# Optimization experiments

Hardware: AMD Instinct MI355X
Metric: run time of the kernel (lower is better)

## Reference

```python
import jax, jax.numpy as jnp
import numpy as np


def setup_inputs() -> dict:
    key = jax.random.key(0)
    ks = jax.random.split(key, 7)
    B, S, D, H = 8, 1024, 1024, 16
    dk = D // H
    return {
        "q": jax.random.normal(ks[0], (B, S, D), dtype=jnp.float32),
        "k": jax.random.normal(ks[1], (B, S, D), dtype=jnp.float32),
        "v": jax.random.normal(ks[2], (B, S, D), dtype=jnp.float32),
        "Wq": jax.random.normal(ks[3], (H, dk, D), dtype=jnp.float32) * 0.03,
        "Wk": jax.random.normal(ks[4], (H, dk, D), dtype=jnp.float32) * 0.03,
        "Wv": jax.random.normal(ks[5], (dk, D), dtype=jnp.float32) * 0.03,
        "Wo": jax.random.normal(ks[6], (D, dk), dtype=jnp.float32) * 0.03,
    }


def reference(q, k, v, Wq, Wk, Wv, Wo):
    # per-head projections (Linear weight layout [out, in]); shared V projection
    dk = Wq.shape[1]
    qs = jnp.einsum("bsd,hed->bhse", q, Wq)          # [B,H,S,dk]
    ks_ = jnp.einsum("btd,hed->bhte", k, Wk)         # [B,H,S,dk]
    vs = jnp.einsum("btd,ed->bte", v, Wv)            # [B,S,dk] shared across heads
    scale = jnp.sqrt(jnp.asarray(dk, dtype=qs.dtype))
    scores = jnp.einsum("bhse,bhte->bhst", qs, ks_) / scale
    attn = jax.nn.softmax(scores, axis=-1)           # [B,H,Sq,Sk]
    heads = jnp.einsum("bhst,bte->bhse", attn, vs)   # [B,H,S,dk]
    head_mean = jnp.mean(heads, axis=1)              # mean over heads -> [B,S,dk]
    outputs = jnp.einsum("bse,de->bsd", head_mean, Wo)
    attn_out = jnp.transpose(attn, (0, 2, 1, 3))     # stacked at dim=2: [B,Sq,H,Sk]
    return outputs, attn_out
```

## Files before the change

### kernel.cpp

```cpp
#include <hip/hip_runtime.h>
#include <hip/hip_bf16.h>


typedef __attribute__((ext_vector_type(4))) float f32x4;
typedef __attribute__((ext_vector_type(8))) short bf16x8;
typedef __attribute__((ext_vector_type(4))) short short4v;
typedef __attribute__((ext_vector_type(2))) unsigned int uint2v;

#define MFMA16(a, b, c) __builtin_amdgcn_mfma_f32_16x16x32_bf16((a), (b), (c), 0, 0, 0)

__device__ __forceinline__ unsigned int rne16(float f) {
  unsigned int u = __float_as_uint(f);
  return u + 0x7fffu + ((u >> 16) & 1u);
}
__device__ __forceinline__ unsigned int pack2bf(float a, float b) {
  return (rne16(a) >> 16) | (rne16(b) & 0xffff0000u);
}
__device__ __forceinline__ short f2bf(float f) {
  return (short)(rne16(f) >> 16);
}
__device__ __forceinline__ float bf2f(short s) {
  return __uint_as_float(((unsigned int)(unsigned short)s) << 16);
}

__global__ __launch_bounds__(256) void proj_qk_kernel(
    const float* __restrict__ qin, const float* __restrict__ kin,
    const float* __restrict__ Wq, const float* __restrict__ Wk,
    __hip_bfloat16* __restrict__ qs, __hip_bfloat16* __restrict__ ks)
{
  const int K = 1024, N = 1024;
  __shared__ short a_lds[128][40];
  __shared__ short b_lds[128][40];
  const int tid  = threadIdx.x;
  const int lane = tid & 63, wid = tid >> 6;
  const int g = lane >> 4, r = lane & 15;
  const bool isK = blockIdx.y >= 8;
  const float* A = isK ? kin : qin;
  const float* W = isK ? Wk : Wq;
  __hip_bfloat16* C = isK ? ks : qs;
  const float scale = isK ? 1.0f : 0.125f;
  const int m0 = blockIdx.x * 128;
  const int n0 = (blockIdx.y & 7) * 128;
  const int wm = (wid >> 1) * 64, wn = (wid & 1) * 64;
  const int lrow = tid >> 3, lcol = (tid & 7) * 4;

  f32x4 acc[4][4];
#pragma unroll
  for (int i = 0; i < 4; ++i)
#pragma unroll
    for (int j = 0; j < 4; ++j) acc[i][j] = (f32x4){0.f, 0.f, 0.f, 0.f};

  for (int k0 = 0; k0 < K; k0 += 32) {
    float4 av[4], wv[4];
#pragma unroll
    for (int p = 0; p < 4; ++p) {
      av[p] = *(const float4*)&A[(m0 + lrow + p * 32) * K + k0 + lcol];
      wv[p] = *(const float4*)&W[(n0 + lrow + p * 32) * K + k0 + lcol];
    }
    __syncthreads();
#pragma unroll
    for (int p = 0; p < 4; ++p) {
      uint2v ua = {pack2bf(av[p].x, av[p].y), pack2bf(av[p].z, av[p].w)};
      uint2v uw = {pack2bf(wv[p].x, wv[p].y), pack2bf(wv[p].z, wv[p].w)};
      *(uint2v*)&a_lds[lrow + p * 32][lcol] = ua;
      *(uint2v*)&b_lds[lrow + p * 32][lcol] = uw;
    }
    __syncthreads();
    bf16x8 af[4], bf[4];
#pragma unroll
    for (int t = 0; t < 4; ++t) {
      af[t] = *(bf16x8*)&a_lds[wm + t * 16 + r][g * 8];
      bf[t] = *(bf16x8*)&b_lds[wn + t * 16 + r][g * 8];
    }
#pragma unroll
    for (int mt = 0; mt < 4; ++mt)
#pragma unroll
      for (int nt = 0; nt < 4; ++nt)
        acc[mt][nt] = MFMA16(af[mt], bf[nt], acc[mt][nt]);
  }

#pragma unroll
  for (int mt = 0; mt < 4; ++mt)
#pragma unroll
    for (int nt = 0; nt < 4; ++nt) {
      const int n = n0 + wn + nt * 16 + r;
#pragma unroll
      for (int j = 0; j < 4; ++j) {
        const int m = m0 + wm + mt * 16 + 4 * g + j;
        C[m * N + n] = __float2bfloat16(acc[mt][nt][j] * scale);
      }
    }
}

__global__ __launch_bounds__(256) void proj_v_kernel(
    const float* __restrict__ vin, const float* __restrict__ Wv,
    __hip_bfloat16* __restrict__ vsT)
{
  const int K = 1024;
  __shared__ short a_lds[128][40];
  __shared__ short b_lds[64][40];
  const int tid  = threadIdx.x;
  const int lane = tid & 63, wid = tid >> 6;
  const int g = lane >> 4, r = lane & 15;
  const int m0 = blockIdx.x * 128;
  const int wm = wid * 32;
  const int lrow = tid >> 3, lcol = (tid & 7) * 4;

  f32x4 acc[2][4];
#pragma unroll
  for (int i = 0; i < 2; ++i)
#pragma unroll
    for (int j = 0; j < 4; ++j) acc[i][j] = (f32x4){0.f, 0.f, 0.f, 0.f};

  for (int k0 = 0; k0 < K; k0 += 32) {
    float4 av[4], wv2[2];
#pragma unroll
    for (int p = 0; p < 4; ++p)
      av[p] = *(const float4*)&vin[(m0 + lrow + p * 32) * K + k0 + lcol];
#pragma unroll
    for (int p = 0; p < 2; ++p)
      wv2[p] = *(const float4*)&Wv[(lrow + p * 32) * K + k0 + lcol];
    __syncthreads();
#pragma unroll
    for (int p = 0; p < 4; ++p) {
      uint2v ua = {pack2bf(av[p].x, av[p].y), pack2bf(av[p].z, av[p].w)};
      *(uint2v*)&a_lds[lrow + p * 32][lcol] = ua;
    }
#pragma unroll
    for (int p = 0; p < 2; ++p) {
      uint2v uw = {pack2bf(wv2[p].x, wv2[p].y), pack2bf(wv2[p].z, wv2[p].w)};
      *(uint2v*)&b_lds[lrow + p * 32][lcol] = uw;
    }
    __syncthreads();
    bf16x8 af[2], bf[4];
#pragma unroll
    for (int t = 0; t < 2; ++t) af[t] = *(bf16x8*)&a_lds[wm + t * 16 + r][g * 8];
#pragma unroll
    for (int t = 0; t < 4; ++t) bf[t] = *(bf16x8*)&b_lds[t * 16 + r][g * 8];
#pragma unroll
    for (int mt = 0; mt < 2; ++mt)
#pragma unroll
      for (int nt = 0; nt < 4; ++nt)
        acc[mt][nt] = MFMA16(af[mt], bf[nt], acc[mt][nt]);
  }

#pragma unroll
  for (int mt = 0; mt < 2; ++mt)
#pragma unroll
    for (int nt = 0; nt < 4; ++nt) {
      const int e = nt * 16 + r;
#pragma unroll
      for (int j = 0; j < 4; ++j) {
        const int m = m0 + wm + mt * 16 + 4 * g + j;
        const int b = m >> 10, t = m & 1023;
        vsT[b * 65536 + e * 1024 + t] = __float2bfloat16(acc[mt][nt][j]);
      }
    }
}

__global__ __launch_bounds__(256, 4) void attn_kernel(
    const __hip_bfloat16* __restrict__ qs_, const __hip_bfloat16* __restrict__ ks_,
    const __hip_bfloat16* __restrict__ vsT_, float* __restrict__ attn_out,
    __hip_bfloat16* __restrict__ heads_)
{
  const int S = 1024, H = 16;
  const int tid = threadIdx.x, lane = tid & 63, kc = tid >> 6;
  const int g = lane >> 4, r = lane & 15;
  const int lin = ((int)blockIdx.x & 7) * 1024 + ((int)blockIdx.x >> 3);
  const int qb = lin & 63, h = (lin >> 6) & 15, b = lin >> 10;
  const int bh = b * H + h;
  const int qrow = qb * 16;

  __shared__ short p_big[4][16][260];
  __shared__ float l_lds[4][16];
  __shared__ float inv_lds[16];
  float (*heads_ov)[16][80] = (float (*)[16][80])p_big;

  const short* qsp = (const short*)qs_;
  const short* ksp = (const short*)ks_;
  const short* vsp = (const short*)vsT_;
  short* headsp = (short*)heads_;

  const int qidx = (b * S + qrow + r) * 1024 + h * 64;
  const bf16x8 qf0 = *(const bf16x8*)&qsp[qidx + g * 8];
  const bf16x8 qf1 = *(const bf16x8*)&qsp[qidx + 32 + g * 8];
  const int kbase = (b * S + kc * 256 + r) * 1024 + h * 64 + g * 8;

  unsigned int pk[32];
  float lsa0 = 0.f, lsa1 = 0.f, lsa2 = 0.f, lsa3 = 0.f;
#pragma unroll
  for (int i = 0; i < 4; ++i) {
    const int t0 = i * 64;
    bf16x8 kf[8];
#pragma unroll
    for (int u = 0; u < 4; ++u) {
      kf[2 * u]     = *(const bf16x8*)&ksp[kbase + (t0 + 16 * u) * 1024];
      kf[2 * u + 1] = *(const bf16x8*)&ksp[kbase + (t0 + 16 * u) * 1024 + 32];
    }
    float es[4];
#pragma unroll
    for (int u = 0; u < 4; ++u) {
      f32x4 s = (f32x4){0.f, 0.f, 0.f, 0.f};
      s = MFMA16(kf[2 * u], qf0, s);
      s = MFMA16(kf[2 * u + 1], qf1, s);
      const float e0 = __expf(s[0]), e1 = __expf(s[1]);
      const float e2 = __expf(s[2]), e3 = __expf(s[3]);
      pk[i * 8 + 2 * u]     = pack2bf(e0, e1);
      pk[i * 8 + 2 * u + 1] = pack2bf(e2, e3);
      es[u] = (e0 + e1) + (e2 + e3);
    }
    lsa0 += es[0]; lsa1 += es[1]; lsa2 += es[2]; lsa3 += es[3];
  }
  float ls = (lsa0 + lsa1) + (lsa2 + lsa3);
  ls += __shfl_xor(ls, 16);
  ls += __shfl_xor(ls, 32);
  if (g == 0) l_lds[kc][r] = ls;
  __syncthreads();
  {
    const float lf = (l_lds[0][r] + l_lds[1][r]) + (l_lds[2][r] + l_lds[3][r]);
    if (kc == 0 && g == 0) inv_lds[r] = 1.f / lf;
  }

#pragma unroll
  for (int j = 0; j < 8; ++j) {
    uint2v w0 = {pk[4 * j + 0], pk[4 * j + 1]};
    uint2v w1 = {pk[4 * j + 2], pk[4 * j + 3]};
    *(uint2v*)&p_big[kc][r][j * 32 + 4 * g] = w0;
    *(uint2v*)&p_big[kc][r][j * 32 + 16 + 4 * g] = w1;
  }
  __syncthreads();

  f32x4 hacc[4];
#pragma unroll
  for (int i = 0; i < 4; ++i) hacc[i] = (f32x4){0.f, 0.f, 0.f, 0.f};
  const int vbase = b * 65536 + r * 1024 + g * 8 + kc * 256;

#pragma unroll
  for (int j = 0; j < 8; ++j) {
    const int tcl = j * 32;
    bf16x8 vf[4];
#pragma unroll
    for (int nt = 0; nt < 4; ++nt)
      vf[nt] = *(const bf16x8*)&vsp[vbase + nt * 16384 + tcl];
    const bf16x8 pa = *(bf16x8*)&p_big[kc][r][tcl + g * 8];
#pragma unroll
    for (int nt = 0; nt < 4; ++nt)
      hacc[nt] = MFMA16(pa, vf[nt], hacc[nt]);
  }

  {
    const int half = lane >> 5, l32 = lane & 31;
#pragma unroll
    for (int rp = 0; rp < 8; ++rp) {
      const int row = rp * 2 + half;
      const bf16x8 pe = *(const bf16x8*)&p_big[kc][row][l32 * 8];
      const float invr = inv_lds[row];
      f32x4 o0, o1;
      o0[0] = bf2f(pe[0]) * invr; o0[1] = bf2f(pe[1]) * invr;
      o0[2] = bf2f(pe[2]) * invr; o0[3] = bf2f(pe[3]) * invr;
      o1[0] = bf2f(pe[4]) * invr; o1[1] = bf2f(pe[5]) * invr;
      o1[2] = bf2f(pe[6]) * invr; o1[3] = bf2f(pe[7]) * invr;
      const int base = ((b * S + qrow + row) * H + h) * S + kc * 256 + l32 * 8;
      __builtin_nontemporal_store(o0, (f32x4*)&attn_out[base]);
      __builtin_nontemporal_store(o1, (f32x4*)&attn_out[base + 4]);
    }
  }
  __syncthreads();

#pragma unroll
  for (int nt = 0; nt < 4; ++nt)
#pragma unroll
    for (int j = 0; j < 4; ++j)
      heads_ov[kc][4 * g + j][nt * 16 + r] = hacc[nt][j];
  __syncthreads();

  {
    const int row = tid >> 4, c4 = (tid & 15) * 4;
    const float invr = inv_lds[row];
    short4v hv;
#pragma unroll
    for (int i = 0; i < 4; ++i) {
      const float s4 = (heads_ov[0][row][c4 + i] + heads_ov[1][row][c4 + i]) +
                       (heads_ov[2][row][c4 + i] + heads_ov[3][row][c4 + i]);
      hv[i] = f2bf(s4 * invr);
    }
    *(short4v*)&headsp[(bh * S + qrow + row) * 64 + c4] = hv;
  }
}

__global__ __launch_bounds__(256) void out_kernel(
    const __hip_bfloat16* __restrict__ heads_, const float* __restrict__ Wo,
    float* __restrict__ out)
{
  __shared__ float hm[16][64];
  const int tid = threadIdx.x;
  const int m0 = blockIdx.x * 16;
  const short* headsp = (const short*)heads_;

  {
    const int row = tid >> 4, e4 = (tid & 15) * 4;
    const int m = m0 + row, b = m >> 10, s = m & 1023;
    float a0 = 0.f, a1 = 0.f, a2 = 0.f, a3 = 0.f;
    for (int hh = 0; hh < 16; ++hh) {
      const short4v hv =
          *(const short4v*)&headsp[((b * 16 + hh) * 1024 + s) * 64 + e4];
      a0 += bf2f(hv[0]); a1 += bf2f(hv[1]); a2 += bf2f(hv[2]); a3 += bf2f(hv[3]);
    }
    const float sc = 1.f / 16.f;
    hm[row][e4 + 0] = a0 * sc; hm[row][e4 + 1] = a1 * sc;
    hm[row][e4 + 2] = a2 * sc; hm[row][e4 + 3] = a3 * sc;
  }
  __syncthreads();

  for (int c = 0; c < 4; ++c) {
    const int d = c * 256 + tid;
    float4 wo4[16];
#pragma unroll
    for (int i = 0; i < 16; ++i) wo4[i] = *(const float4*)&Wo[d * 64 + i * 4];
    for (int row = 0; row < 16; ++row) {
      float a = 0.f;
#pragma unroll
      for (int i = 0; i < 16; ++i) {
        const float4 h4 = *(const float4*)&hm[row][i * 4];
        a += h4.x * wo4[i].x + h4.y * wo4[i].y + h4.z * wo4[i].z + h4.w * wo4[i].w;
      }
      out[(m0 + row) * 1024 + d] = a;
    }
  }
}

extern "C" void kernel_launch(void* const* d_in, const int* in_sizes, int n_in,
                              void* d_out, int out_size, void* d_ws, size_t ws_size,
                              hipStream_t stream) {
  const float* q  = (const float*)d_in[0];
  const float* k  = (const float*)d_in[1];
  const float* v  = (const float*)d_in[2];
  const float* Wq = (const float*)d_in[3];
  const float* Wk = (const float*)d_in[4];
  const float* Wv = (const float*)d_in[5];
  const float* Wo = (const float*)d_in[6];

  float* out0 = (float*)d_out;
  float* attn = out0 + (size_t)8 * 1024 * 1024;

  char* ws = (char*)d_ws;
  __hip_bfloat16* qs    = (__hip_bfloat16*)(ws);
  __hip_bfloat16* ksbuf = (__hip_bfloat16*)(ws + (16u << 20));
  __hip_bfloat16* vsT   = (__hip_bfloat16*)(ws + (32u << 20));
  __hip_bfloat16* heads = (__hip_bfloat16*)(ws + (33u << 20));

  dim3 blk(256);
  proj_qk_kernel<<<dim3(64, 16), blk, 0, stream>>>(q, k, Wq, Wk, qs, ksbuf);
  proj_v_kernel<<<dim3(64), blk, 0, stream>>>(v, Wv, vsT);
  attn_kernel<<<dim3(8192), blk, 0, stream>>>(qs, ksbuf, vsT, attn, heads);
  out_kernel<<<dim3(512), blk, 0, stream>>>(heads, Wo, out0);
}
```

Measured before the change: 426.3 us.

## Pre-convert Q/K inputs and weights to bf16 and load GEMM tiles via global_load_lds

Adds a separate conversion kernel that writes bf16 copies of q, k, Wq and Wk to the workspace. The QK projection GEMM then streams those bf16 tiles straight into LDS with global_load_lds, replacing the register round trip and in-kernel conversion. The goal is to halve the bytes the GEMM reads on each pass and to cut VALU and LDS-store work in its inner loop. The cost is an extra pass that reads all fp32 inputs and writes bf16 copies, the loss of LDS row padding (bank conflicts possible), and a qbuf that overlaps the heads buffer, which is safe only because the launches run in order.

```diff
diff --git a/kernel.cpp b/kernel.cpp
--- a/kernel.cpp
+++ b/kernel.cpp
@@ -5,9 +5,15 @@
 typedef __attribute__((ext_vector_type(4))) float f32x4;
 typedef __attribute__((ext_vector_type(8))) short bf16x8;
 typedef __attribute__((ext_vector_type(4))) short short4v;
+typedef __attribute__((ext_vector_type(4))) unsigned int uint4v;
 typedef __attribute__((ext_vector_type(2))) unsigned int uint2v;
 
 #define MFMA16(a, b, c) __builtin_amdgcn_mfma_f32_16x16x32_bf16((a), (b), (c), 0, 0, 0)
+
+#define GLL16(gp, lp)                                                          \
+  __builtin_amdgcn_global_load_lds(                                            \
+      (const __attribute__((address_space(1))) void*)(gp),                     \
+      (__attribute__((address_space(3))) void*)(lp), 16, 0, 0)
 
 __device__ __forceinline__ unsigned int rne16(float f) {
   unsigned int u = __float_as_uint(f);
@@ -23,26 +29,51 @@
   return __uint_as_float(((unsigned int)(unsigned short)s) << 16);
 }
 
+__global__ __launch_bounds__(256) void cvt_kernel(
+    const float* __restrict__ q, const float* __restrict__ k,
+    const float* __restrict__ Wq, const float* __restrict__ Wk,
+    short* __restrict__ qb, short* __restrict__ kb,
+    short* __restrict__ Wqb, short* __restrict__ Wkb)
+{
+  const int y = blockIdx.y;
+  const float* src = (y == 0) ? q : (y == 1) ? k : (y == 2) ? Wq : Wk;
+  short* dst = (y == 0) ? qb : (y == 1) ? kb : (y == 2) ? Wqb : Wkb;
+  const int n = (y < 2) ? (8 * 1024 * 1024) : (1024 * 1024);
+  const int i = (blockIdx.x * 256 + threadIdx.x) * 8;
+  if (i >= n) return;
+  const float4 a = *(const float4*)&src[i];
+  const float4 b = *(const float4*)&src[i + 4];
+  uint4v o = {pack2bf(a.x, a.y), pack2bf(a.z, a.w),
+              pack2bf(b.x, b.y), pack2bf(b.z, b.w)};
+  *(uint4v*)&dst[i] = o;
+}
+
 __global__ __launch_bounds__(256) void proj_qk_kernel(
-    const float* __restrict__ qin, const float* __restrict__ kin,
-    const float* __restrict__ Wq, const float* __restrict__ Wk,
+    const short* __restrict__ qb, const short* __restrict__ kb,
+    const short* __restrict__ Wqb, const short* __restrict__ Wkb,
     __hip_bfloat16* __restrict__ qs, __hip_bfloat16* __restrict__ ks)
 {
   const int K = 1024, N = 1024;
-  __shared__ short a_lds[128][40];
-  __shared__ short b_lds[128][40];
-  const int tid  = threadIdx.x;
+  __shared__ short a_lds[128 * 32];
+  __shared__ short b_lds[128 * 32];
+  const int tid = threadIdx.x;
   const int lane = tid & 63, wid = tid >> 6;
   const int g = lane >> 4, r = lane & 15;
   const bool isK = blockIdx.y >= 8;
-  const float* A = isK ? kin : qin;
-  const float* W = isK ? Wk : Wq;
+  const short* A = isK ? kb : qb;
+  const short* W = isK ? Wkb : Wqb;
   __hip_bfloat16* C = isK ? ks : qs;
   const float scale = isK ? 1.0f : 0.125f;
   const int m0 = blockIdx.x * 128;
   const int n0 = (blockIdx.y & 7) * 128;
   const int wm = (wid >> 1) * 64, wn = (wid & 1) * 64;
-  const int lrow = tid >> 3, lcol = (tid & 7) * 4;
+
+  const int Ra = wid * 32;
+  const int srow = lane >> 2, sslot = lane & 3;
+  const long aoff0 = (long)(m0 + Ra + srow) * K + sslot * 8;
+  const long aoff1 = (long)(m0 + Ra + 16 + srow) * K + sslot * 8;
+  const long boff0 = (long)(n0 + Ra + srow) * K + sslot * 8;
+  const long boff1 = (long)(n0 + Ra + 16 + srow) * K + sslot * 8;
 
   f32x4 acc[4][4];
 #pragma unroll
@@ -51,26 +82,17 @@
     for (int j = 0; j < 4; ++j) acc[i][j] = (f32x4){0.f, 0.f, 0.f, 0.f};
 
   for (int k0 = 0; k0 < K; k0 += 32) {
-    float4 av[4], wv[4];
-#pragma unroll
-    for (int p = 0; p < 4; ++p) {
-      av[p] = *(const float4*)&A[(m0 + lrow + p * 32) * K + k0 + lcol];
-      wv[p] = *(const float4*)&W[(n0 + lrow + p * 32) * K + k0 + lcol];
-    }
     __syncthreads();
-#pragma unroll
-    for (int p = 0; p < 4; ++p) {
-      uint2v ua = {pack2bf(av[p].x, av[p].y), pack2bf(av[p].z, av[p].w)};
-      uint2v uw = {pack2bf(wv[p].x, wv[p].y), pack2bf(wv[p].z, wv[p].w)};
-      *(uint2v*)&a_lds[lrow + p * 32][lcol] = ua;
-      *(uint2v*)&b_lds[lrow + p * 32][lcol] = uw;
-    }
+    GLL16(A + aoff0 + k0, &a_lds[Ra * 32]);
+    GLL16(A + aoff1 + k0, &a_lds[(Ra + 16) * 32]);
+    GLL16(W + boff0 + k0, &b_lds[Ra * 32]);
+    GLL16(W + boff1 + k0, &b_lds[(Ra + 16) * 32]);
     __syncthreads();
     bf16x8 af[4], bf[4];
 #pragma unroll
     for (int t = 0; t < 4; ++t) {
-      af[t] = *(bf16x8*)&a_lds[wm + t * 16 + r][g * 8];
-      bf[t] = *(bf16x8*)&b_lds[wn + t * 16 + r][g * 8];
+      af[t] = *(bf16x8*)&a_lds[(wm + t * 16 + r) * 32 + g * 8];
+      bf[t] = *(bf16x8*)&b_lds[(wn + t * 16 + r) * 32 + g * 8];
     }
 #pragma unroll
     for (int mt = 0; mt < 4; ++mt)
@@ -348,9 +370,16 @@
   __hip_bfloat16* ksbuf = (__hip_bfloat16*)(ws + (16u << 20));
   __hip_bfloat16* vsT   = (__hip_bfloat16*)(ws + (32u << 20));
   __hip_bfloat16* heads = (__hip_bfloat16*)(ws + (33u << 20));
+  short* qbuf  = (short*)(ws + (33u << 20));
+  short* kbuf  = (short*)(ws + (49u << 20));
+  short* Wqbuf = (short*)(ws + (65u << 20));
+  short* Wkbuf = (short*)(ws + (67u << 20));
 
   dim3 blk(256);
-  proj_qk_kernel<<<dim3(64, 16), blk, 0, stream>>>(q, k, Wq, Wk, qs, ksbuf);
+  cvt_kernel<<<dim3(4096, 4), blk, 0, stream>>>(q, k, Wq, Wk,
+                                                qbuf, kbuf, Wqbuf, Wkbuf);
+  proj_qk_kernel<<<dim3(64, 16), blk, 0, stream>>>(qbuf, kbuf, Wqbuf, Wkbuf,
+                                                   qs, ksbuf);
   proj_v_kernel<<<dim3(64), blk, 0, stream>>>(v, Wv, vsT);
   attn_kernel<<<dim3(8192), blk, 0, stream>>>(qs, ksbuf, vsT, attn, heads);
   out_kernel<<<dim3(512), blk, 0, stream>>>(heads, Wo, out0);
```

Result: no change. 421.5 us (-1.1%).
